# Kernel tuning notes

Measured on AMD Instinct MI355X. Metric: run time of the kernel, lower is better.

## Reference

```python
import jax, jax.numpy as jnp
import numpy as np

IN_FEATURES = 2048
OUT_FEATURES = 2048
BATCH = 4096


def setup_inputs() -> dict:
    key = jax.random.key(0)
    kx, kw, kb, kp = jax.random.split(key, 4)
    x = jax.random.normal(kx, (BATCH, IN_FEATURES), dtype=jnp.float32)
    weight = jax.random.normal(kw, (OUT_FEATURES, IN_FEATURES), dtype=jnp.float32)
    bias = jax.random.normal(kb, (OUT_FEATURES,), dtype=jnp.float32)
    # torch uses torch.randperm(in_features) at forward time; we fix a permutation here
    indices = jax.random.permutation(kp, IN_FEATURES).astype(jnp.int64)
    return {"x": x, "weight": weight, "bias": bias, "indices": indices}


def reference(x, weight, bias, indices):
    # Original: (x[:, None, :] * weight)[:, :, indices].sum(dim=2) + bias
    # Summing the permuted reduction axis == contracting the permuted operands;
    # we gather both x and weight along the permutation then do a real GEMM,
    # avoiding the huge [B, out, in] intermediate while keeping identical math.
    xp = x[:, indices]            # [B, in]
    wp = weight[:, indices]       # [out, in]
    return jnp.einsum('bi,oi->bo', xp, wp) + bias[None, :]
```

## Files before the change

### kernel.cpp

```cpp
#include <hip/hip_runtime.h>
#include <hip/hip_bf16.h>

#define M_DIM 4096
#define N_DIM 2048
#define K_DIM 2048

typedef __bf16 bf16x8 __attribute__((ext_vector_type(8)));
typedef float f32x4 __attribute__((ext_vector_type(4)));
typedef unsigned short u16x8 __attribute__((ext_vector_type(8)));

__device__ __forceinline__ unsigned short f32_to_bf16_rne(float f) {
  unsigned int u = __float_as_uint(f);
  u += 0x7fffu + ((u >> 16) & 1u);
  return (unsigned short)(u >> 16);
}

__global__ __launch_bounds__(256) void cvt_f32_to_bf16(
    const float* __restrict__ in, unsigned short* __restrict__ out, int n8) {
  int i = blockIdx.x * 256 + threadIdx.x;
  if (i >= n8) return;
  const f32x4* p = reinterpret_cast<const f32x4*>(in) + (size_t)i * 2;
  f32x4 a = p[0];
  f32x4 b = p[1];
  u16x8 o;
  o[0] = f32_to_bf16_rne(a[0]);
  o[1] = f32_to_bf16_rne(a[1]);
  o[2] = f32_to_bf16_rne(a[2]);
  o[3] = f32_to_bf16_rne(a[3]);
  o[4] = f32_to_bf16_rne(b[0]);
  o[5] = f32_to_bf16_rne(b[1]);
  o[6] = f32_to_bf16_rne(b[2]);
  o[7] = f32_to_bf16_rne(b[3]);
  reinterpret_cast<u16x8*>(out)[i] = o;
}

__device__ __forceinline__ void gload_lds16(const unsigned short* g, unsigned short* l) {
  __builtin_amdgcn_global_load_lds(
      (const __attribute__((address_space(1))) unsigned int*)g,
      (__attribute__((address_space(3))) unsigned int*)l, 16, 0, 0);
}

#define BM 128
#define BN 128
#define BK 32

__global__ __launch_bounds__(256) void gemm_bf16_bt(
    const unsigned short* __restrict__ A,
    const unsigned short* __restrict__ B,
    const float* __restrict__ bias,
    float* __restrict__ C) {
  __shared__ unsigned short As[BM * BK];
  __shared__ unsigned short Bs[BN * BK];

  const int tid  = threadIdx.x;
  const int lane = tid & 63;
  const int wave = tid >> 6;
  const int wr   = wave >> 1;
  const int wc   = wave & 1;
  const int bn   = blockIdx.x;
  const int bm   = blockIdx.y;

  const int lrow = tid >> 2;
  const int lcol = (tid & 3) * 8;

  const unsigned short* a0 = A + (size_t)(bm * BM + lrow) * K_DIM + lcol;
  const unsigned short* a1 = a0 + (size_t)64 * K_DIM;
  const unsigned short* b0 = B + (size_t)(bn * BN + lrow) * K_DIM + lcol;
  const unsigned short* b1 = b0 + (size_t)64 * K_DIM;

  unsigned short* asd0 = &As[tid * 8];
  unsigned short* asd1 = &As[2048 + tid * 8];
  unsigned short* bsd0 = &Bs[tid * 8];
  unsigned short* bsd1 = &Bs[2048 + tid * 8];

  const int fr = lane & 15;
  const int kg = (lane >> 4) * 8;

  const f32x4 z = {0.f, 0.f, 0.f, 0.f};
  f32x4 acc[4][4];
#pragma unroll
  for (int i = 0; i < 4; ++i)
#pragma unroll
    for (int j = 0; j < 4; ++j) acc[i][j] = z;

  for (int k0 = 0; k0 < K_DIM; k0 += BK) {
    __syncthreads();
    gload_lds16(a0 + k0, asd0);
    gload_lds16(a1 + k0, asd1);
    gload_lds16(b0 + k0, bsd0);
    gload_lds16(b1 + k0, bsd1);
    __syncthreads();

    bf16x8 af[4], bfr[4];
#pragma unroll
    for (int mi = 0; mi < 4; ++mi)
      af[mi] = *reinterpret_cast<const bf16x8*>(&As[(wr * 64 + mi * 16 + fr) * BK + kg]);
#pragma unroll
    for (int ni = 0; ni < 4; ++ni)
      bfr[ni] = *reinterpret_cast<const bf16x8*>(&Bs[(wc * 64 + ni * 16 + fr) * BK + kg]);

#pragma unroll
    for (int mi = 0; mi < 4; ++mi)
#pragma unroll
      for (int ni = 0; ni < 4; ++ni)
        acc[mi][ni] = __builtin_amdgcn_mfma_f32_16x16x32_bf16(af[mi], bfr[ni], acc[mi][ni], 0, 0, 0);
  }

  const int orow0 = bm * BM + wr * 64 + (lane >> 4) * 4;
  const int ocol0 = bn * BN + wc * 64 + (lane & 15);
#pragma unroll
  for (int ni = 0; ni < 4; ++ni) {
    const int col = ocol0 + ni * 16;
    const float bv = bias[col];
#pragma unroll
    for (int mi = 0; mi < 4; ++mi) {
      const f32x4 v = acc[mi][ni];
      const int row = orow0 + mi * 16;
#pragma unroll
      for (int r = 0; r < 4; ++r)
        C[(size_t)(row + r) * N_DIM + col] = v[r] + bv;
    }
  }
}

__global__ __launch_bounds__(256) void gemm_f32_naive(
    const float* __restrict__ X, const float* __restrict__ W,
    const float* __restrict__ bias, float* __restrict__ C) {
  int o = blockIdx.x * 256 + threadIdx.x;
  if (o >= M_DIM * N_DIM) return;
  int m = o / N_DIM, n = o % N_DIM;
  const float* xr = X + (size_t)m * K_DIM;
  const float* wr = W + (size_t)n * K_DIM;
  float s = 0.f;
  for (int k = 0; k < K_DIM; ++k) s += xr[k] * wr[k];
  C[o] = s + bias[n];
}

extern "C" void kernel_launch(void* const* d_in, const int* in_sizes, int n_in,
                              void* d_out, int out_size, void* d_ws, size_t ws_size,
                              hipStream_t stream) {
  const float* x    = (const float*)d_in[0];
  const float* w    = (const float*)d_in[1];
  const float* bias = (const float*)d_in[2];
  float* out = (float*)d_out;

  const size_t x_elems = (size_t)M_DIM * K_DIM;
  const size_t w_elems = (size_t)N_DIM * K_DIM;
  const size_t need = (x_elems + w_elems) * sizeof(unsigned short);

  if (ws_size < need) {
    gemm_f32_naive<<<(M_DIM * N_DIM + 255) / 256, 256, 0, stream>>>(x, w, bias, out);
    return;
  }

  unsigned short* xb = (unsigned short*)d_ws;
  unsigned short* wb = xb + x_elems;

  cvt_f32_to_bf16<<<(int)(x_elems / 8 / 256), 256, 0, stream>>>(x, xb, (int)(x_elems / 8));
  cvt_f32_to_bf16<<<(int)(w_elems / 8 / 256), 256, 0, stream>>>(w, wb, (int)(w_elems / 8));

  dim3 grid(N_DIM / BN, M_DIM / BM);
  gemm_bf16_bt<<<grid, 256, 0, stream>>>(xb, wb, bias, out);
}
```

Baseline: 65.15 us.

## Pipeline GEMM with triple-buffered LDS, XOR swizzle, 8 waves, merged conversion

Rewrites the bf16 GEMM to use 256x128x64 tiles with 8 waves per block. A three-stage LDS ring is filled by async global-to-LDS loads that are interleaved with MFMA groups, with waits based on vmcnt and s_setprio around the MFMA bursts. LDS chunks are XOR-swizzled so fragment reads avoid bank conflicts. The two fp32-to-bf16 conversion launches are merged into one. The aim is to hide global load latency, cut the per-iteration barriers, and reduce launch overhead, at the cost of more LDS, register pressure, and fragile hand-placed scheduling.

```diff
diff --git a/kernel.cpp b/kernel.cpp
--- a/kernel.cpp
+++ b/kernel.cpp
@@ -4,6 +4,13 @@
 #define M_DIM 4096
 #define N_DIM 2048
 #define K_DIM 2048
+
+#define BM 256
+#define BN 128
+#define BK 64
+#define NT (K_DIM / BK)
+#define A_TILE (BM * BK)
+#define B_TILE (BN * BK)
 
 typedef __bf16 bf16x8 __attribute__((ext_vector_type(8)));
 typedef float f32x4 __attribute__((ext_vector_type(4)));
@@ -15,22 +22,20 @@
   return (unsigned short)(u >> 16);
 }
 
-__global__ __launch_bounds__(256) void cvt_f32_to_bf16(
-    const float* __restrict__ in, unsigned short* __restrict__ out, int n8) {
+__global__ __launch_bounds__(256) void cvt_both(
+    const float* __restrict__ x, const float* __restrict__ w,
+    unsigned short* __restrict__ out, int xn8, int totn8) {
   int i = blockIdx.x * 256 + threadIdx.x;
-  if (i >= n8) return;
-  const f32x4* p = reinterpret_cast<const f32x4*>(in) + (size_t)i * 2;
-  f32x4 a = p[0];
-  f32x4 b = p[1];
+  if (i >= totn8) return;
+  const float* src = (i < xn8) ? (x + (size_t)i * 8)
+                               : (w + (size_t)(i - xn8) * 8);
+  f32x4 a = reinterpret_cast<const f32x4*>(src)[0];
+  f32x4 b = reinterpret_cast<const f32x4*>(src)[1];
   u16x8 o;
-  o[0] = f32_to_bf16_rne(a[0]);
-  o[1] = f32_to_bf16_rne(a[1]);
-  o[2] = f32_to_bf16_rne(a[2]);
-  o[3] = f32_to_bf16_rne(a[3]);
-  o[4] = f32_to_bf16_rne(b[0]);
-  o[5] = f32_to_bf16_rne(b[1]);
-  o[6] = f32_to_bf16_rne(b[2]);
-  o[7] = f32_to_bf16_rne(b[3]);
+  o[0] = f32_to_bf16_rne(a[0]); o[1] = f32_to_bf16_rne(a[1]);
+  o[2] = f32_to_bf16_rne(a[2]); o[3] = f32_to_bf16_rne(a[3]);
+  o[4] = f32_to_bf16_rne(b[0]); o[5] = f32_to_bf16_rne(b[1]);
+  o[6] = f32_to_bf16_rne(b[2]); o[7] = f32_to_bf16_rne(b[3]);
   reinterpret_cast<u16x8*>(out)[i] = o;
 }
 
@@ -40,17 +45,15 @@
       (__attribute__((address_space(3))) unsigned int*)l, 16, 0, 0);
 }
 
-#define BM 128
-#define BN 128
-#define BK 32
-
-__global__ __launch_bounds__(256) void gemm_bf16_bt(
+#define LD8(p) (*reinterpret_cast<const bf16x8*>(p))
+
+__global__ __launch_bounds__(512, 2) void gemm_8w(
     const unsigned short* __restrict__ A,
     const unsigned short* __restrict__ B,
     const float* __restrict__ bias,
     float* __restrict__ C) {
-  __shared__ unsigned short As[BM * BK];
-  __shared__ unsigned short Bs[BN * BK];
+  __shared__ unsigned short As[3 * A_TILE];
+  __shared__ unsigned short Bs[3 * B_TILE];
 
   const int tid  = threadIdx.x;
   const int lane = tid & 63;
@@ -60,21 +63,47 @@
   const int bn   = blockIdx.x;
   const int bm   = blockIdx.y;
 
-  const int lrow = tid >> 2;
-  const int lcol = (tid & 3) * 8;
-
-  const unsigned short* a0 = A + (size_t)(bm * BM + lrow) * K_DIM + lcol;
-  const unsigned short* a1 = a0 + (size_t)64 * K_DIM;
-  const unsigned short* b0 = B + (size_t)(bn * BN + lrow) * K_DIM + lcol;
-  const unsigned short* b1 = b0 + (size_t)64 * K_DIM;
-
-  unsigned short* asd0 = &As[tid * 8];
-  unsigned short* asd1 = &As[2048 + tid * 8];
-  unsigned short* bsd0 = &Bs[tid * 8];
-  unsigned short* bsd1 = &Bs[2048 + tid * 8];
+  const int srow   = tid >> 3;
+  const int schunk = (tid & 7) ^ (srow & 7);
+  const unsigned short* Ag[4];
+  const unsigned short* Bg[2];
+#pragma unroll
+  for (int j = 0; j < 4; ++j)
+    Ag[j] = A + (size_t)(bm * BM + j * 64 + srow) * K_DIM + schunk * 8;
+#pragma unroll
+  for (int j = 0; j < 2; ++j)
+    Bg[j] = B + (size_t)(bn * BN + j * 64 + srow) * K_DIM + schunk * 8;
+
+#define STAGE_A01(buf, k0) do { \
+    unsigned short* _d = &As[(buf) * A_TILE + tid * 8]; \
+    gload_lds16(Ag[0] + (k0), _d); \
+    gload_lds16(Ag[1] + (k0), _d + 4096); \
+  } while (0)
+#define STAGE_A23(buf, k0) do { \
+    unsigned short* _d = &As[(buf) * A_TILE + 8192 + tid * 8]; \
+    gload_lds16(Ag[2] + (k0), _d); \
+    gload_lds16(Ag[3] + (k0), _d + 4096); \
+  } while (0)
+#define STAGE_B01(buf, k0) do { \
+    unsigned short* _d = &Bs[(buf) * B_TILE + tid * 8]; \
+    gload_lds16(Bg[0] + (k0), _d); \
+    gload_lds16(Bg[1] + (k0), _d + 4096); \
+  } while (0)
 
   const int fr = lane & 15;
-  const int kg = (lane >> 4) * 8;
+  const int qq = lane >> 4;
+  const int xr = fr & 7;
+  int aoff[4][2], boff[4][2];
+#pragma unroll
+  for (int mi = 0; mi < 4; ++mi)
+#pragma unroll
+    for (int kk = 0; kk < 2; ++kk)
+      aoff[mi][kk] = ((wr * 64 + mi * 16 + fr) * 8 + ((kk * 4 + qq) ^ xr)) * 8;
+#pragma unroll
+  for (int ni = 0; ni < 4; ++ni)
+#pragma unroll
+    for (int kk = 0; kk < 2; ++kk)
+      boff[ni][kk] = ((wc * 64 + ni * 16 + fr) * 8 + ((kk * 4 + qq) ^ xr)) * 8;
 
   const f32x4 z = {0.f, 0.f, 0.f, 0.f};
   f32x4 acc[4][4];
@@ -83,44 +112,85 @@
 #pragma unroll
     for (int j = 0; j < 4; ++j) acc[i][j] = z;
 
-  for (int k0 = 0; k0 < K_DIM; k0 += BK) {
-    __syncthreads();
-    gload_lds16(a0 + k0, asd0);
-    gload_lds16(a1 + k0, asd1);
-    gload_lds16(b0 + k0, bsd0);
-    gload_lds16(b1 + k0, bsd1);
-    __syncthreads();
-
-    bf16x8 af[4], bfr[4];
-#pragma unroll
-    for (int mi = 0; mi < 4; ++mi)
-      af[mi] = *reinterpret_cast<const bf16x8*>(&As[(wr * 64 + mi * 16 + fr) * BK + kg]);
-#pragma unroll
-    for (int ni = 0; ni < 4; ++ni)
-      bfr[ni] = *reinterpret_cast<const bf16x8*>(&Bs[(wc * 64 + ni * 16 + fr) * BK + kg]);
-
-#pragma unroll
-    for (int mi = 0; mi < 4; ++mi)
-#pragma unroll
-      for (int ni = 0; ni < 4; ++ni)
-        acc[mi][ni] = __builtin_amdgcn_mfma_f32_16x16x32_bf16(af[mi], bfr[ni], acc[mi][ni], 0, 0, 0);
+#define MFMA_ROW(mi, av) do { \
+    acc[mi][0] = __builtin_amdgcn_mfma_f32_16x16x32_bf16(av, bv0, acc[mi][0], 0, 0, 0); \
+    acc[mi][1] = __builtin_amdgcn_mfma_f32_16x16x32_bf16(av, bv1, acc[mi][1], 0, 0, 0); \
+    acc[mi][2] = __builtin_amdgcn_mfma_f32_16x16x32_bf16(av, bv2, acc[mi][2], 0, 0, 0); \
+    acc[mi][3] = __builtin_amdgcn_mfma_f32_16x16x32_bf16(av, bv3, acc[mi][3], 0, 0, 0); \
+  } while (0)
+
+#define BODY(t_, STG) do { \
+    const int b_ = (t_) % 3; \
+    const unsigned short* Asb = &As[b_ * A_TILE]; \
+    const unsigned short* Bsb = &Bs[b_ * B_TILE]; \
+    const int sb_ = ((t_) + 2) % 3; \
+    const int sk0_ = ((t_) + 2) * BK; \
+    bf16x8 av0, av1, av2, av3, bv0, bv1, bv2, bv3; \
+     \
+    bv0 = LD8(Bsb + boff[0][0]); bv1 = LD8(Bsb + boff[1][0]); \
+    bv2 = LD8(Bsb + boff[2][0]); bv3 = LD8(Bsb + boff[3][0]); \
+    av0 = LD8(Asb + aoff[0][0]); av1 = LD8(Asb + aoff[1][0]); \
+    if (STG) STAGE_A01(sb_, sk0_); \
+    __builtin_amdgcn_s_setprio(1); \
+    MFMA_ROW(0, av0); MFMA_ROW(1, av1); \
+    __builtin_amdgcn_s_setprio(0); \
+    av2 = LD8(Asb + aoff[2][0]); av3 = LD8(Asb + aoff[3][0]); \
+    if (STG) STAGE_A23(sb_, sk0_); \
+    __builtin_amdgcn_s_setprio(1); \
+    MFMA_ROW(2, av2); MFMA_ROW(3, av3); \
+    __builtin_amdgcn_s_setprio(0); \
+     \
+    bv0 = LD8(Bsb + boff[0][1]); bv1 = LD8(Bsb + boff[1][1]); \
+    bv2 = LD8(Bsb + boff[2][1]); bv3 = LD8(Bsb + boff[3][1]); \
+    av0 = LD8(Asb + aoff[0][1]); av1 = LD8(Asb + aoff[1][1]); \
+    if (STG) STAGE_B01(sb_, sk0_); \
+    __builtin_amdgcn_s_setprio(1); \
+    MFMA_ROW(0, av0); MFMA_ROW(1, av1); \
+    __builtin_amdgcn_s_setprio(0); \
+    av2 = LD8(Asb + aoff[2][1]); av3 = LD8(Asb + aoff[3][1]); \
+    __builtin_amdgcn_s_setprio(1); \
+    MFMA_ROW(2, av2); MFMA_ROW(3, av3); \
+    __builtin_amdgcn_s_setprio(0); \
+  } while (0)
+
+  STAGE_A01(0, 0); STAGE_A23(0, 0); STAGE_B01(0, 0);
+  STAGE_A01(1, BK); STAGE_A23(1, BK); STAGE_B01(1, BK);
+  asm volatile("s_waitcnt vmcnt(6)" ::: "memory");
+  __builtin_amdgcn_s_barrier();
+  __builtin_amdgcn_sched_barrier(0);
+
+#pragma unroll 1
+  for (int t = 0; t < NT - 2; ++t) {
+    BODY(t, 1);
+    asm volatile("s_waitcnt vmcnt(6)" ::: "memory");
+    __builtin_amdgcn_s_barrier();
+    __builtin_amdgcn_sched_barrier(0);
   }
-
-  const int orow0 = bm * BM + wr * 64 + (lane >> 4) * 4;
-  const int ocol0 = bn * BN + wc * 64 + (lane & 15);
+  BODY(NT - 2, 0);
+  asm volatile("s_waitcnt vmcnt(0)" ::: "memory");
+  __builtin_amdgcn_s_barrier();
+  __builtin_amdgcn_sched_barrier(0);
+  BODY(NT - 1, 0);
+
+  const int orow0 = bm * BM + wr * 64 + qq * 4;
+  const int ocol0 = bn * BN + wc * 64 + fr;
 #pragma unroll
   for (int ni = 0; ni < 4; ++ni) {
     const int col = ocol0 + ni * 16;
     const float bv = bias[col];
 #pragma unroll
     for (int mi = 0; mi < 4; ++mi) {
-      const f32x4 v = acc[mi][ni];
       const int row = orow0 + mi * 16;
 #pragma unroll
       for (int r = 0; r < 4; ++r)
-        C[(size_t)(row + r) * N_DIM + col] = v[r] + bv;
+        C[(size_t)(row + r) * N_DIM + col] = acc[mi][ni][r] + bv;
     }
   }
+#undef BODY
+#undef MFMA_ROW
+#undef STAGE_A01
+#undef STAGE_A23
+#undef STAGE_B01
 }
 
 __global__ __launch_bounds__(256) void gemm_f32_naive(
@@ -156,9 +226,10 @@
   unsigned short* xb = (unsigned short*)d_ws;
   unsigned short* wb = xb + x_elems;
 
-  cvt_f32_to_bf16<<<(int)(x_elems / 8 / 256), 256, 0, stream>>>(x, xb, (int)(x_elems / 8));
-  cvt_f32_to_bf16<<<(int)(w_elems / 8 / 256), 256, 0, stream>>>(w, wb, (int)(w_elems / 8));
+  const int xn8 = (int)(x_elems / 8);
+  const int totn8 = (int)((x_elems + w_elems) / 8);
+  cvt_both<<<(totn8 + 255) / 256, 256, 0, stream>>>(x, w, xb, xn8, totn8);
 
   dim3 grid(N_DIM / BN, M_DIM / BM);
-  gemm_bf16_bt<<<grid, 256, 0, stream>>>(xb, wb, bias, out);
-}
+  gemm_8w<<<grid, 512, 0, stream>>>(xb, wb, bias, out);
+}
```

After: 62.09 us. -4.7%, faster.

## Pre-swizzle bf16 operands into MFMA fragment layout and load directly to registers

Applied to the files above, without the earlier changes.

The conversion kernel now writes X and W in a chunked layout where each 16x32 tile is stored in the exact per-lane order the 16x16x32 MFMA expects, and both conversions are merged into a single launch. The GEMM drops LDS staging and barriers entirely: each wave loads its fragments straight from global memory into registers with a double-buffered ping-pong over K. A remapped 1D grid groups workgroups for L2 locality, and launch bounds request two blocks per CU. The risk is that without LDS sharing, each wave re-reads its operands from global/L2, which raises L2 traffic, and the double register sets increase register pressure.

```diff
diff --git a/kernel.cpp b/kernel.cpp
--- a/kernel.cpp
+++ b/kernel.cpp
@@ -4,6 +4,8 @@
 #define M_DIM 4096
 #define N_DIM 2048
 #define K_DIM 2048
+#define K32   (K_DIM / 32)
+
 
 typedef __bf16 bf16x8 __attribute__((ext_vector_type(8)));
 typedef float f32x4 __attribute__((ext_vector_type(4)));
@@ -15,66 +17,56 @@
   return (unsigned short)(u >> 16);
 }
 
-__global__ __launch_bounds__(256) void cvt_f32_to_bf16(
-    const float* __restrict__ in, unsigned short* __restrict__ out, int n8) {
-  int i = blockIdx.x * 256 + threadIdx.x;
-  if (i >= n8) return;
-  const f32x4* p = reinterpret_cast<const f32x4*>(in) + (size_t)i * 2;
-  f32x4 a = p[0];
-  f32x4 b = p[1];
+__global__ __launch_bounds__(256) void cvt_chunk(
+    const float* __restrict__ x, const float* __restrict__ w,
+    unsigned short* __restrict__ outx, unsigned short* __restrict__ outw,
+    int xslots, int totslots) {
+  int s = blockIdx.x * 256 + threadIdx.x;
+  if (s >= totslots) return;
+  const float* in;
+  unsigned short* out;
+  int ls = s;
+  if (s < xslots) { in = x; out = outx; }
+  else            { in = w; out = outw; ls = s - xslots; }
+  const int chunk = ls >> 6, l = ls & 63;
+  const int rb = chunk >> 6, kb = chunk & 63;
+  const size_t off = (size_t)(rb * 16 + (l & 15)) * K_DIM + kb * 32 + (l >> 4) * 8;
+  f32x4 a = *reinterpret_cast<const f32x4*>(in + off);
+  f32x4 b = *reinterpret_cast<const f32x4*>(in + off + 4);
   u16x8 o;
-  o[0] = f32_to_bf16_rne(a[0]);
-  o[1] = f32_to_bf16_rne(a[1]);
-  o[2] = f32_to_bf16_rne(a[2]);
-  o[3] = f32_to_bf16_rne(a[3]);
-  o[4] = f32_to_bf16_rne(b[0]);
-  o[5] = f32_to_bf16_rne(b[1]);
-  o[6] = f32_to_bf16_rne(b[2]);
-  o[7] = f32_to_bf16_rne(b[3]);
-  reinterpret_cast<u16x8*>(out)[i] = o;
+  o[0] = f32_to_bf16_rne(a[0]); o[1] = f32_to_bf16_rne(a[1]);
+  o[2] = f32_to_bf16_rne(a[2]); o[3] = f32_to_bf16_rne(a[3]);
+  o[4] = f32_to_bf16_rne(b[0]); o[5] = f32_to_bf16_rne(b[1]);
+  o[6] = f32_to_bf16_rne(b[2]); o[7] = f32_to_bf16_rne(b[3]);
+  reinterpret_cast<u16x8*>(out)[ls] = o;
 }
 
-__device__ __forceinline__ void gload_lds16(const unsigned short* g, unsigned short* l) {
-  __builtin_amdgcn_global_load_lds(
-      (const __attribute__((address_space(1))) unsigned int*)g,
-      (__attribute__((address_space(3))) unsigned int*)l, 16, 0, 0);
-}
+#define LD8(p) (*reinterpret_cast<const bf16x8*>(p))
 
-#define BM 128
-#define BN 128
-#define BK 32
-
-__global__ __launch_bounds__(256) void gemm_bf16_bt(
-    const unsigned short* __restrict__ A,
-    const unsigned short* __restrict__ B,
+__global__ __launch_bounds__(256, 2) void gemm_reg(
+    const unsigned short* __restrict__ Ac,
+    const unsigned short* __restrict__ Bc,
     const float* __restrict__ bias,
     float* __restrict__ C) {
-  __shared__ unsigned short As[BM * BK];
-  __shared__ unsigned short Bs[BN * BK];
-
   const int tid  = threadIdx.x;
   const int lane = tid & 63;
   const int wave = tid >> 6;
   const int wr   = wave >> 1;
   const int wc   = wave & 1;
-  const int bn   = blockIdx.x;
-  const int bm   = blockIdx.y;
 
-  const int lrow = tid >> 2;
-  const int lcol = (tid & 3) * 8;
+  const int orig = blockIdx.x;
+  const int wgid = (orig & 7) * 64 + (orig >> 3);
+  const int bn = wgid >> 5;
+  const int bm = wgid & 31;
 
-  const unsigned short* a0 = A + (size_t)(bm * BM + lrow) * K_DIM + lcol;
-  const unsigned short* a1 = a0 + (size_t)64 * K_DIM;
-  const unsigned short* b0 = B + (size_t)(bn * BN + lrow) * K_DIM + lcol;
-  const unsigned short* b1 = b0 + (size_t)64 * K_DIM;
-
-  unsigned short* asd0 = &As[tid * 8];
-  unsigned short* asd1 = &As[2048 + tid * 8];
-  unsigned short* bsd0 = &Bs[tid * 8];
-  unsigned short* bsd1 = &Bs[2048 + tid * 8];
-
-  const int fr = lane & 15;
-  const int kg = (lane >> 4) * 8;
+  const unsigned short* pa[4];
+  const unsigned short* pb[4];
+#pragma unroll
+  for (int mi = 0; mi < 4; ++mi)
+    pa[mi] = Ac + (size_t)(bm * 8 + wr * 4 + mi) * K32 * 512 + lane * 8;
+#pragma unroll
+  for (int ni = 0; ni < 4; ++ni)
+    pb[ni] = Bc + (size_t)(bn * 8 + wc * 4 + ni) * K32 * 512 + lane * 8;
 
   const f32x4 z = {0.f, 0.f, 0.f, 0.f};
   f32x4 acc[4][4];
@@ -83,44 +75,61 @@
 #pragma unroll
     for (int j = 0; j < 4; ++j) acc[i][j] = z;
 
-  for (int k0 = 0; k0 < K_DIM; k0 += BK) {
-    __syncthreads();
-    gload_lds16(a0 + k0, asd0);
-    gload_lds16(a1 + k0, asd1);
-    gload_lds16(b0 + k0, bsd0);
-    gload_lds16(b1 + k0, bsd1);
-    __syncthreads();
+  bf16x8 aX[4][2], bX[4][2], aY[4][2], bY[4][2];
 
-    bf16x8 af[4], bfr[4];
-#pragma unroll
-    for (int mi = 0; mi < 4; ++mi)
-      af[mi] = *reinterpret_cast<const bf16x8*>(&As[(wr * 64 + mi * 16 + fr) * BK + kg]);
-#pragma unroll
-    for (int ni = 0; ni < 4; ++ni)
-      bfr[ni] = *reinterpret_cast<const bf16x8*>(&Bs[(wc * 64 + ni * 16 + fr) * BK + kg]);
+#define LOADSET(aS, bS) do { \
+    _Pragma("unroll") \
+    for (int mi = 0; mi < 4; ++mi) { \
+      aS[mi][0] = LD8(pa[mi]); aS[mi][1] = LD8(pa[mi] + 512); pa[mi] += 1024; \
+    } \
+    _Pragma("unroll") \
+    for (int ni = 0; ni < 4; ++ni) { \
+      bS[ni][0] = LD8(pb[ni]); bS[ni][1] = LD8(pb[ni] + 512); pb[ni] += 1024; \
+    } \
+  } while (0)
 
-#pragma unroll
-    for (int mi = 0; mi < 4; ++mi)
-#pragma unroll
-      for (int ni = 0; ni < 4; ++ni)
-        acc[mi][ni] = __builtin_amdgcn_mfma_f32_16x16x32_bf16(af[mi], bfr[ni], acc[mi][ni], 0, 0, 0);
+#define MFMASET(aS, bS) do { \
+    _Pragma("unroll") \
+    for (int kk = 0; kk < 2; ++kk) \
+      _Pragma("unroll") \
+      for (int mi = 0; mi < 4; ++mi) { \
+        acc[mi][0] = __builtin_amdgcn_mfma_f32_16x16x32_bf16(aS[mi][kk], bS[0][kk], acc[mi][0], 0, 0, 0); \
+        acc[mi][1] = __builtin_amdgcn_mfma_f32_16x16x32_bf16(aS[mi][kk], bS[1][kk], acc[mi][1], 0, 0, 0); \
+        acc[mi][2] = __builtin_amdgcn_mfma_f32_16x16x32_bf16(aS[mi][kk], bS[2][kk], acc[mi][2], 0, 0, 0); \
+        acc[mi][3] = __builtin_amdgcn_mfma_f32_16x16x32_bf16(aS[mi][kk], bS[3][kk], acc[mi][3], 0, 0, 0); \
+      } \
+  } while (0)
+
+  LOADSET(aX, bX);
+#pragma unroll 1
+  for (int p = 0; p < 15; ++p) {
+    LOADSET(aY, bY);
+    MFMASET(aX, bX);
+    LOADSET(aX, bX);
+    MFMASET(aY, bY);
   }
+  LOADSET(aY, bY);
+  MFMASET(aX, bX);
+  MFMASET(aY, bY);
 
-  const int orow0 = bm * BM + wr * 64 + (lane >> 4) * 4;
-  const int ocol0 = bn * BN + wc * 64 + (lane & 15);
+  const int fr = lane & 15;
+  const int qq = lane >> 4;
+  const int orow0 = bm * 128 + wr * 64 + qq * 4;
+  const int ocol0 = bn * 128 + wc * 64 + fr;
 #pragma unroll
   for (int ni = 0; ni < 4; ++ni) {
     const int col = ocol0 + ni * 16;
     const float bv = bias[col];
 #pragma unroll
     for (int mi = 0; mi < 4; ++mi) {
-      const f32x4 v = acc[mi][ni];
       const int row = orow0 + mi * 16;
 #pragma unroll
       for (int r = 0; r < 4; ++r)
-        C[(size_t)(row + r) * N_DIM + col] = v[r] + bv;
+        C[(size_t)(row + r) * N_DIM + col] = acc[mi][ni][r] + bv;
     }
   }
+#undef MFMASET
+#undef LOADSET
 }
 
 __global__ __launch_bounds__(256) void gemm_f32_naive(
@@ -156,9 +165,9 @@
   unsigned short* xb = (unsigned short*)d_ws;
   unsigned short* wb = xb + x_elems;
 
-  cvt_f32_to_bf16<<<(int)(x_elems / 8 / 256), 256, 0, stream>>>(x, xb, (int)(x_elems / 8));
-  cvt_f32_to_bf16<<<(int)(w_elems / 8 / 256), 256, 0, stream>>>(w, wb, (int)(w_elems / 8));
+  const int xslots = (int)(x_elems / 8);
+  const int totslots = (int)((x_elems + w_elems) / 8);
+  cvt_chunk<<<(totslots + 255) / 256, 256, 0, stream>>>(x, w, xb, wb, xslots, totslots);
 
-  dim3 grid(N_DIM / BN, M_DIM / BM);
-  gemm_bf16_bt<<<grid, 256, 0, stream>>>(xb, wb, bias, out);
+  gemm_reg<<<512, 256, 0, stream>>>(xb, wb, bias, out);
 }
```

Measured after the change: 60.84 us. -6.6%, faster.
